# Kernel tuning notes

Hardware: AMD Instinct MI355X
Metric: run time of the kernel (lower is better)

The kernel has to match this reference:

```python
import jax, jax.numpy as jnp
import numpy as np
import math

B, T, D, S, V = 128, 32, 64, 32, 8192
MAX_REC = 8
PONDER = 0.01
TWO_PI = 2.0 * math.pi


def setup_inputs():
    key = jax.random.key(0)
    ks = jax.random.split(key, 12)
    sd = 1.0 / math.sqrt(D)
    g = lambda k, shape, s: jax.random.normal(k, shape, jnp.float32) * s
    return {
        "x_seq": jax.random.randint(ks[0], (B, T), 0, V),
        "encoder_emb": g(ks[1], (V, 2 * D), 0.02),
        "vq_emb": g(ks[2], (V, 2 * D), sd),
        "norm_rg": jnp.ones((D,), jnp.float32), "norm_rb": jnp.zeros((D,), jnp.float32),
        "norm_ig": jnp.ones((D,), jnp.float32), "norm_ib": jnp.zeros((D,), jnp.float32),
        "qkv_Wr": g(ks[3], (3, D, D), sd), "qkv_br": g(ks[4], (3, D), sd),
        "qkv_Wi": g(ks[5], (3, D, D), sd), "qkv_bi": g(ks[6], (3, D), sd),
        "gate_w": g(ks[7], (2 * D,), sd), "gate_b": jnp.zeros((), jnp.float32),
        "arb_W": g(ks[8], (3, 2 * D), sd), "arb_b": jnp.zeros((3,), jnp.float32),
        "dec_W": g(ks[9], (V, 2 * D), sd), "dec_b": jnp.zeros((V,), jnp.float32),
        "halt_bias": jnp.asarray(3.0, jnp.float32),
        "input_gate": jnp.asarray(0.0, jnp.float32),
    }


def _ln(x, g, b, eps=1e-5):
    mu = x.mean(-1, keepdims=True)
    var = ((x - mu) ** 2).mean(-1, keepdims=True)
    return (x - mu) * jax.lax.rsqrt(var + eps) * g + b


def _forward(x_seq, encoder_emb, vq_emb, norm_rg, norm_rb, norm_ig, norm_ib,
             qkv_Wr, qkv_br, qkv_Wi, qkv_bi, gate_w, gate_b, arb_W, arb_b,
             dec_W, dec_b, halt_bias, input_gate):
    sg = jax.lax.stop_gradient
    e_sq = (vq_emb ** 2).sum(-1)  # [V]
    alpha = jax.nn.sigmoid(input_gate)
    bias = jax.nn.softplus(halt_bias)

    def clin(xr, xi, Wr, br, Wi, bi):
        # torch ComplexLinear: real = fc_r(xr) - fc_i(xi); imag = fc_r(xi) + fc_i(xr)
        return (xr @ Wr.T + br) - (xi @ Wi.T + bi), (xi @ Wr.T + br) + (xr @ Wi.T + bi)

    def mem_write(gr, gi, mr, mi):
        flat = jnp.concatenate([gr, gi], -1)
        wg = jax.nn.sigmoid(flat @ gate_w + gate_b)[:, None, None]  # [B,1,1]
        shr, shi = jnp.roll(mr, 1, axis=1), jnp.roll(mi, 1, axis=1)
        hr = wg * gr[:, None, :] + (1.0 - wg) * shr[:, :1]
        hi = wg * gi[:, None, :] + (1.0 - wg) * shi[:, :1]
        return jnp.concatenate([hr, shr[:, 1:]], 1), jnp.concatenate([hi, shi[:, 1:]], 1)

    def time_step(carry, xt):
        gw_r, gw_i, mem_r, mem_i = carry
        x_r, x_i = xt
        gw_r = alpha * gw_r + (1.0 - alpha) * x_r
        gw_i = alpha * gw_i + (1.0 - alpha) * x_i
        active = jnp.ones((B,), jnp.float32)
        acc_vq = jnp.zeros((B,), jnp.float32)
        acc_ent = jnp.zeros((B,), jnp.float32)
        acc_pond = jnp.zeros((B,), jnp.float32)
        acc_ph = jnp.zeros((B,), jnp.float32)
        fin_idx = jnp.zeros((B,), jnp.int32)
        prev_ang = jnp.arctan2(gw_i, gw_r)
        for _ in range(MAX_REC):
            cr = _ln(gw_r, norm_rg, norm_rb)
            ci = _ln(gw_i, norm_ig, norm_ib)
            z_flat = jnp.concatenate([cr, ci], -1)  # [B,2D]
            # squared-euclidean scores; argmin identical to cdist argmin
            d2 = (z_flat ** 2).sum(-1, keepdims=True) - 2.0 * (z_flat @ vq_emb.T) + e_sq
            idx = jnp.argmin(d2, -1).astype(jnp.int32)
            z_q = vq_emb[idx]
            vq_loss = ((z_q - sg(z_flat)) ** 2).mean(-1) + 0.25 * ((sg(z_q) - z_flat) ** 2).mean(-1)
            z_st = z_flat + sg(z_q - z_flat)  # straight-through
            counts = jnp.zeros((V,), jnp.float32).at[idx].add(1.0) / B
            entropy = -(counts * jnp.log(counts + 1e-10)).sum()
            v_r, v_i = z_st[:, :D], z_st[:, D:]
            # Hermitian gating
            qr, qi = clin(cr, ci, qkv_Wr[0], qkv_br[0], qkv_Wi[0], qkv_bi[0])
            kr, ki = clin(cr, ci, qkv_Wr[1], qkv_br[1], qkv_Wi[1], qkv_bi[1])
            vr2, vi2 = clin(cr, ci, qkv_Wr[2], qkv_br[2], qkv_Wi[2], qkv_bi[2])
            gate = jax.nn.sigmoid((qr * kr + qi * ki).sum(-1, keepdims=True))
            g_r, g_i = vr2 * gate, vi2 * gate
            # memory read (Re<m, q> attention over slots)
            sim = jnp.einsum('bsd,bd->bs', mem_r, cr) + jnp.einsum('bsd,bd->bs', mem_i, ci)
            attn = jax.nn.softmax(sim, -1)
            m_r = jnp.einsum('bs,bsd->bd', attn, mem_r)
            m_i = jnp.einsum('bs,bsd->bd', attn, mem_i)
            gates = jax.nn.softmax(z_flat @ arb_W.T + arb_b, -1)  # [B,3]
            upd_r = gates[:, 0:1] * g_r + gates[:, 1:2] * m_r + gates[:, 2:3] * v_r
            upd_i = gates[:, 0:1] * g_i + gates[:, 1:2] * m_i + gates[:, 2:3] * v_i
            cand_r = 0.6 * cr + 0.4 * upd_r
            cand_i = 0.6 * ci + 0.4 * upd_i
            ang = jnp.arctan2(cand_i, cand_r)
            diff = jnp.abs(ang - prev_ang)
            diff = jnp.minimum(diff, TWO_PI - diff)
            acc_ph = acc_ph + active * diff.mean(-1)
            prev_ang = ang
            halt_prob = jax.nn.sigmoid(bias - vq_loss)
            should_stop = (halt_prob > 0.5).astype(jnp.float32)
            acc_pond = acc_pond + active * PONDER
            mflat = active > 0.5
            acc_vq = jnp.where(mflat, vq_loss, acc_vq)
            acc_ent = jnp.where(mflat, entropy, acc_ent)
            fin_idx = jnp.where(mflat, idx, fin_idx)
            am = mflat[:, None]
            gw_r = jnp.where(am, cand_r, gw_r)
            gw_i = jnp.where(am, cand_i, gw_i)
            active = active * (1.0 - should_stop)
        mem_r, mem_i = mem_write(gw_r, gw_i, mem_r, mem_i)
        stats_t = jnp.stack([acc_vq.mean(), acc_ent.mean(), acc_pond.mean(), acc_ph.mean()])
        return (gw_r, gw_i, mem_r, mem_i), (gw_r, gw_i, fin_idx, stats_t)

    emb = encoder_emb[x_seq]  # [B,T,2D]
    xr = jnp.transpose(emb[..., :D], (1, 0, 2))  # [T,B,D]
    xi = jnp.transpose(emb[..., D:], (1, 0, 2))
    init = (jnp.zeros((B, D), jnp.float32), jnp.zeros((B, D), jnp.float32),
            jnp.zeros((B, S, D), jnp.float32), jnp.zeros((B, S, D), jnp.float32))
    _, (out_r, out_i, idxs, stats) = jax.lax.scan(time_step, init, (xr, xi))
    out = jnp.concatenate([jnp.transpose(out_r, (1, 0, 2)),
                           jnp.transpose(out_i, (1, 0, 2))], -1)  # [B,T,2D]
    logits = out @ dec_W.T + dec_b  # [B,T,V]
    return logits, stats.sum(0) / T, jnp.transpose(idxs)  # [B,T]


def reference(x_seq, encoder_emb, vq_emb, norm_rg, norm_rb, norm_ig, norm_ib, qkv_Wr, qkv_br, qkv_Wi, qkv_bi, gate_w, gate_b, arb_W, arb_b, dec_W, dec_b, halt_bias, input_gate):
    return _forward(x_seq, encoder_emb, vq_emb, norm_rg, norm_rb, norm_ig, norm_ib,
                    qkv_Wr, qkv_br, qkv_Wi, qkv_bi, gate_w, gate_b, arb_W, arb_b,
                    dec_W, dec_b, halt_bias, input_gate)
```

## Files before the change

kernel.cpp:

```cpp
#include <hip/hip_runtime.h>
#include <math.h>

#define TT 32
#define MAXREC 8
#define NBLK 256
#define NTHR 512

#define OFF_ZBUF   0u
#define OFF_KEYS   65536u
#define OFF_ZDONE  196608u
#define OFF_SDONE  198656u
#define OFF_OUTHB  200704u
#define OFF_RST    1249280u
#define OFF_DWB    1251328u

#define SENT 0x7FFFFFFFu
#define LOGN 33554432u
#define TWO_PI_F 6.283185307179586f

typedef float f32x4 __attribute__((ext_vector_type(4)));
typedef short bf16x8 __attribute__((ext_vector_type(8)));
typedef unsigned long long u64;

__device__ __forceinline__ float wredsum(float v) {
#pragma unroll
  for (int m = 32; m > 0; m >>= 1) v += __shfl_xor(v, m);
  return v;
}

__device__ __forceinline__ u64 shflx64(u64 v, int m) {
  int lo = __shfl_xor((int)(unsigned)(v & 0xffffffffull), m);
  int hi = __shfl_xor((int)(unsigned)(v >> 32), m);
  return ((u64)(unsigned)hi << 32) | (unsigned)lo;
}

__device__ __forceinline__ u64 packkey(float d, unsigned c) {
  unsigned u = __float_as_uint(d);
  u = (u & 0x80000000u) ? ~u : (u | 0x80000000u);
  return ((u64)u << 32) | c;
}
__device__ __forceinline__ float unpackd2(u64 key) {
  unsigned hi = (unsigned)(key >> 32);
  unsigned orig = (hi & 0x80000000u) ? (hi & 0x7fffffffu) : ~hi;
  return __uint_as_float(orig);
}
__device__ __forceinline__ unsigned short f2bf(float f) {
  unsigned u = __float_as_uint(f);
  unsigned r = (u >> 16) & 1u;
  u += 0x7fffu + r;
  return (unsigned short)(u >> 16);
}

__device__ __forceinline__ unsigned ld_coh32(const unsigned* p) {
  unsigned v;
  asm volatile("global_load_dword %0, %1, off sc0 sc1\n\ts_waitcnt vmcnt(0)"
               : "=&v"(v) : "v"(p) : "memory");
  return v;
}
__device__ __forceinline__ void st_coh_f32(float* p, float v) {
  asm volatile("global_store_dword %0, %1, off sc0 sc1" :: "v"(p), "v"(v) : "memory");
}
__device__ __forceinline__ void st_coh32(unsigned* p, unsigned v) {
  asm volatile("global_store_dword %0, %1, off sc0 sc1" :: "v"(p), "v"(v) : "memory");
}
__device__ __forceinline__ void st_coh64(u64* p, u64 v) {
  asm volatile("global_store_dwordx2 %0, %1, off sc0 sc1" :: "v"(p), "v"(v) : "memory");
}
__device__ __forceinline__ void drain_vm() {
  asm volatile("s_waitcnt vmcnt(0)" ::: "memory");
}

__device__ __forceinline__ void ld8w(const float* base,
    unsigned o0, unsigned o1, unsigned o2, unsigned o3,
    unsigned o4, unsigned o5, unsigned o6, unsigned o7,
    f32x4& a0, f32x4& a1, f32x4& a2, f32x4& a3,
    f32x4& a4, f32x4& a5, f32x4& a6, f32x4& a7) {
  asm volatile(
      "global_load_dwordx4 %0, %8, %16 sc0 sc1\n\t"
      "global_load_dwordx4 %1, %9, %16 sc0 sc1\n\t"
      "global_load_dwordx4 %2, %10, %16 sc0 sc1\n\t"
      "global_load_dwordx4 %3, %11, %16 sc0 sc1\n\t"
      "global_load_dwordx4 %4, %12, %16 sc0 sc1\n\t"
      "global_load_dwordx4 %5, %13, %16 sc0 sc1\n\t"
      "global_load_dwordx4 %6, %14, %16 sc0 sc1\n\t"
      "global_load_dwordx4 %7, %15, %16 sc0 sc1\n\t"
      "s_waitcnt vmcnt(0)"
      : "=&v"(a0), "=&v"(a1), "=&v"(a2), "=&v"(a3),
        "=&v"(a4), "=&v"(a5), "=&v"(a6), "=&v"(a7)
      : "v"(o0), "v"(o1), "v"(o2), "v"(o3),
        "v"(o4), "v"(o5), "v"(o6), "v"(o7),
        "s"(base)
      : "memory");
}
__device__ __forceinline__ void ld8x2_issue(const char* base,
    unsigned o0, unsigned o1, unsigned o2, unsigned o3,
    unsigned o4, unsigned o5, unsigned o6, unsigned o7,
    u64& a0, u64& a1, u64& a2, u64& a3, u64& a4, u64& a5, u64& a6, u64& a7) {
  asm volatile(
      "global_load_dwordx2 %0, %8, %16 sc0 sc1\n\t"
      "global_load_dwordx2 %1, %9, %16 sc0 sc1\n\t"
      "global_load_dwordx2 %2, %10, %16 sc0 sc1\n\t"
      "global_load_dwordx2 %3, %11, %16 sc0 sc1\n\t"
      "global_load_dwordx2 %4, %12, %16 sc0 sc1\n\t"
      "global_load_dwordx2 %5, %13, %16 sc0 sc1\n\t"
      "global_load_dwordx2 %6, %14, %16 sc0 sc1\n\t"
      "global_load_dwordx2 %7, %15, %16 sc0 sc1"
      : "=&v"(a0), "=&v"(a1), "=&v"(a2), "=&v"(a3),
        "=&v"(a4), "=&v"(a5), "=&v"(a6), "=&v"(a7)
      : "v"(o0), "v"(o1), "v"(o2), "v"(o3),
        "v"(o4), "v"(o5), "v"(o6), "v"(o7),
        "s"(base)
      : "memory");
}

__global__ __launch_bounds__(512) void sacrsn_init(char* __restrict__ ws) {
  unsigned* zd = (unsigned*)(ws + OFF_ZDONE);
  unsigned* sd = (unsigned*)(ws + OFF_SDONE);
  zd[threadIdx.x] = 0u;
  sd[threadIdx.x] = 0u;
}

__global__ __launch_bounds__(256) void k_prep(const float* __restrict__ dW,
                                              char* __restrict__ ws) {
  unsigned short* dWb = (unsigned short*)(ws + OFF_DWB);
  const int i = (blockIdx.x * 256 + threadIdx.x) * 4;
  float4 v = *(const float4*)(dW + i);
  ushort4 o;
  o.x = f2bf(v.x); o.y = f2bf(v.y); o.z = f2bf(v.z); o.w = f2bf(v.w);
  *(ushort4*)(dWb + i) = o;
}

__global__ __launch_bounds__(NTHR) void sacrsn_main(
    const int* __restrict__ x_seq, const float* __restrict__ enc,
    const float* __restrict__ vqe,
    const float* __restrict__ nrg, const float* __restrict__ nrb,
    const float* __restrict__ nig, const float* __restrict__ nib,
    const float* __restrict__ qWr, const float* __restrict__ qbr,
    const float* __restrict__ qWi, const float* __restrict__ qbi,
    const float* __restrict__ gtw, const float* __restrict__ gtb,
    const float* __restrict__ aW, const float* __restrict__ ab,
    const float* __restrict__ hbp, const float* __restrict__ igp,
    float* __restrict__ dout, char* __restrict__ ws)
{
  float* zbuf = (float*)(ws + OFF_ZBUF);
  u64*   keys = (u64*)(ws + OFF_KEYS);
  unsigned* zdone = (unsigned*)(ws + OFF_ZDONE);
  unsigned* sdone = (unsigned*)(ws + OFF_SDONE);
  unsigned short* outhB = (unsigned short*)(ws + OFF_OUTHB);
  float* rst  = (float*)(ws + OFF_RST);

  const int tid = threadIdx.x;
  const int wv = tid >> 6, ln = tid & 63;
  const int blk = blockIdx.x;
  const bool owner = (blk < 128);

  __shared__ float els[64 * 128];
  __shared__ float zloc[128 * 128];
  __shared__ u64 vtmp[128 * 17];
  __shared__ float esqL[64];
  __shared__ float z2locL[128];
  __shared__ float memLr[32 * 65];
  __shared__ float memLi[32 * 65];
  __shared__ float gwrowL[128], pangL[64], zfmL[128], zqL[128];
  __shared__ float qkL[6][64], simL[32], attnL[32], mrL[64], miL[64];
  __shared__ unsigned idxL[128] __attribute__((aligned(16)));
  __shared__ u64 key128L[128];
  __shared__ float arbWL[3 * 128];
  __shared__ float scalL[8], entpL[2], vqpL[2], wsumL[2];
  __shared__ float accL[4], totL[4];
  __shared__ float dmeanS;
  __shared__ u64 actM[2], actN[2];
  __shared__ unsigned pollOK, pollSent, mfS;

  const float alpha = 1.0f / (1.0f + expf(-igp[0]));
  const float onema = 1.0f - alpha;
  const float hbias = log1pf(expf(hbp[0]));
  const float gtb0 = gtb[0];

  if (!owner) {
    const int s = blk - 128;
#pragma unroll
    for (int j = 0; j < 4; ++j) {
      int f4 = tid + j * NTHR;
      int c = f4 >> 5, k4 = f4 & 31;
      float4 v = *(const float4*)&vqe[((size_t)(s * 64 + c) << 7) + (k4 << 2)];
      *(float4*)&els[(c << 7) + ((k4 ^ (c & 31)) << 2)] = v;
    }
    __syncthreads();
    if (tid < 64) {
      float sm = 0.0f;
#pragma unroll 8
      for (int k4 = 0; k4 < 32; ++k4) {
        float4 v = *(const float4*)&els[(tid << 7) + ((k4 ^ (tid & 31)) << 2)];
        sm = fmaf(v.x, v.x, fmaf(v.y, v.y, fmaf(v.z, v.z, fmaf(v.w, v.w, sm))));
      }
      esqL[tid] = sm;
    }
    __syncthreads();
    unsigned k = 0;
    while (true) {
      bool done = false;
      while (true) {
        if (tid == 0) { pollOK = 1u; pollSent = 1u; }
        __syncthreads();
        if (tid < 128) {
          unsigned v = ld_coh32(&zdone[tid * 4]);
          if ((int)(v - (k + 1u)) < 0) pollOK = 0u;
          if (v != SENT) pollSent = 0u;
        }
        __syncthreads();
        if (pollSent) { done = true; break; }
        if (pollOK) break;
        __builtin_amdgcn_s_sleep(1);
      }
      if (done) break;
      {
        f32x4 a0, a1, a2, a3, a4, a5, a6, a7;
        const unsigned tb = (unsigned)tid * 16u;
        ld8w(zbuf, tb, tb + 8192u, tb + 16384u, tb + 24576u,
             tb + 32768u, tb + 40960u, tb + 49152u, tb + 57344u,
             a0, a1, a2, a3, a4, a5, a6, a7);
        __builtin_amdgcn_sched_barrier(0);
        f32x4 va[8] = {a0, a1, a2, a3, a4, a5, a6, a7};
#pragma unroll
        for (int u = 0; u < 8; ++u) {
          int f4 = u * NTHR + tid;
          int row = f4 >> 5, k4 = f4 & 31;
          *(f32x4*)&zloc[(row << 7) + ((k4 ^ (row & 31)) << 2)] = va[u];
        }
      }
      __syncthreads();
      if (tid < 128) {
        float sm = 0.0f;
#pragma unroll 8
        for (int k4 = 0; k4 < 32; ++k4) {
          float4 q = *(const float4*)&zloc[(tid << 7) + ((k4 ^ (tid & 31)) << 2)];
          sm = fmaf(q.x, q.x, fmaf(q.y, q.y, fmaf(q.z, q.z, fmaf(q.w, q.w, sm))));
        }
        z2locL[tid] = sm;
      }
      const int rt = tid & 31, ct = tid >> 5;
      float acc[4][4];
#pragma unroll
      for (int rr = 0; rr < 4; ++rr)
#pragma unroll
        for (int cc = 0; cc < 4; ++cc) acc[rr][cc] = 0.0f;
#pragma unroll 2
      for (int k4 = 0; k4 < 32; ++k4) {
        float4 zv[4], ev[4];
#pragma unroll
        for (int rr = 0; rr < 4; ++rr)
          zv[rr] = *(const float4*)&zloc[((rt + rr * 32) << 7) + ((k4 ^ rt) << 2)];
#pragma unroll
        for (int cc = 0; cc < 4; ++cc) {
          int cl = ct * 4 + cc;
          ev[cc] = *(const float4*)&els[(cl << 7) + ((k4 ^ (cl & 31)) << 2)];
        }
#pragma unroll
        for (int rr = 0; rr < 4; ++rr)
#pragma unroll
          for (int cc = 0; cc < 4; ++cc)
            acc[rr][cc] = fmaf(zv[rr].x, ev[cc].x, fmaf(zv[rr].y, ev[cc].y,
                          fmaf(zv[rr].z, ev[cc].z, fmaf(zv[rr].w, ev[cc].w, acc[rr][cc]))));
      }
      __syncthreads();
#pragma unroll
      for (int rr = 0; rr < 4; ++rr) {
        const int row = rt + rr * 32;
        const float z2r = z2locL[row];
        u64 key = ~0ull;
#pragma unroll
        for (int cc = 0; cc < 4; ++cc) {
          int cl = ct * 4 + cc;
          float d2 = (z2r - 2.0f * acc[rr][cc]) + esqL[cl];
          u64 pk = packkey(d2, (unsigned)(s * 64 + cl));
          if (pk < key) key = pk;
        }
        vtmp[row * 17 + ct] = key;
      }
      __syncthreads();
      if (tid < 128) {
        u64 kmin = vtmp[tid * 17];
#pragma unroll
        for (int w = 1; w < 16; ++w) { u64 o = vtmp[tid * 17 + w]; if (o < kmin) kmin = o; }
        st_coh64(&keys[(size_t)s * 128 + tid], kmin);
      }
      drain_vm();
      __syncthreads();
      if (tid == 0) st_coh32(&sdone[s * 4], k + 1u);
      k++;
    }
    return;
  }

  float lnG = 0.0f, lnB = 0.0f, gtwv = 0.0f;
  if (tid < 64) { lnG = nrg[tid]; lnB = nrb[tid]; }
  else if (tid < 128) { lnG = nig[tid - 64]; lnB = nib[tid - 64]; }
  if (tid < 128) gtwv = gtw[tid];
  for (int i = tid; i < 32 * 65; i += NTHR) { memLr[i] = 0.0f; memLi[i] = 0.0f; }
  if (tid < 4) { totL[tid] = 0.0f; accL[tid] = 0.0f; }
  if (tid < 2) actM[tid] = ~0ull;
  for (int i = tid; i < 384; i += NTHR) arbWL[i] = aW[i];
  {
    int tok = x_seq[blk * TT];
    if (tid < 128) gwrowL[tid] = onema * enc[((size_t)tok << 7) + tid];
  }
  __syncthreads();
  if (tid < 64) pangL[tid] = atan2f(gwrowL[64 + tid], gwrowL[tid]);
  if (tid < 128) {
    float val = gwrowL[tid];
    float mu = wredsum(val) * 0.015625f;
    float xc = val - mu;
    float vr = wredsum(xc * xc) * 0.015625f;
    float z = xc * (1.0f / sqrtf(vr + 1e-5f)) * lnG + lnB;
    zfmL[tid] = z;
    st_coh_f32(&zbuf[(blk << 7) + tid], z);
  }
  drain_vm();
  __syncthreads();
  if (tid == 0) st_coh32(&zdone[blk * 4], 1u);

  int t = 0, it = 0;
  unsigned k = 0;
  for (;;) {
    float encN = 0.0f;
    {
      int tnext = (t + 1 < TT) ? t + 1 : t;
      if (tid < 128) {
        int tk = x_seq[blk * TT + tnext];
        encN = enc[((size_t)tk << 7) + tid];
      }
    }
    if (tid < 192) {
      const int h = tid >> 6, j = tid & 63;
      const float* wr = qWr + h * 4096 + j * 64;
      const float* wi = qWi + h * 4096 + j * 64;
      float da = 0.0f, db_ = 0.0f, dc = 0.0f, de = 0.0f;
#pragma unroll 4
      for (int d4 = 0; d4 < 64; d4 += 4) {
        float4 wrv = *(const float4*)&wr[d4];
        float4 wiv = *(const float4*)&wi[d4];
        float4 crv = *(const float4*)&zfmL[d4];
        float4 civ = *(const float4*)&zfmL[64 + d4];
        da = fmaf(crv.x, wrv.x, fmaf(crv.y, wrv.y, fmaf(crv.z, wrv.z, fmaf(crv.w, wrv.w, da))));
        db_ = fmaf(civ.x, wiv.x, fmaf(civ.y, wiv.y, fmaf(civ.z, wiv.z, fmaf(civ.w, wiv.w, db_))));
        dc = fmaf(civ.x, wrv.x, fmaf(civ.y, wrv.y, fmaf(civ.z, wrv.z, fmaf(civ.w, wrv.w, dc))));
        de = fmaf(crv.x, wiv.x, fmaf(crv.y, wiv.y, fmaf(crv.z, wiv.z, fmaf(crv.w, wiv.w, de))));
      }
      float brv = qbr[h * 64 + j], biv = qbi[h * 64 + j];
      qkL[2 * h][j] = da + brv - db_ - biv;
      qkL[2 * h + 1][j] = dc + brv + de + biv;
    } else if (tid < 224) {
      const int s2 = tid - 192;
      float a2 = 0.0f;
      for (int d = 0; d < 64; ++d)
        a2 = fmaf(memLr[s2 * 65 + d], zfmL[d], fmaf(memLi[s2 * 65 + d], zfmL[64 + d], a2));
      simL[s2] = a2;
    } else if (tid < 227) {
      const int h = tid - 224;
      float a2 = ab[h];
      for (int k2 = 0; k2 < 128; ++k2) a2 = fmaf(zfmL[k2], arbWL[h * 128 + k2], a2);
      scalL[3 + h] = a2;
    }
    __syncthreads();
    if (tid < 64) {
      float p = fmaf(qkL[0][tid], qkL[2][tid], qkL[1][tid] * qkL[3][tid]);
      p = wredsum(p);
      if (tid == 0) scalL[0] = 1.0f / (1.0f + expf(-p));
    } else if (tid < 96) {
      const int s2 = tid - 64;
      float v = simL[s2];
      float m = v;
#pragma unroll
      for (int msk = 16; msk > 0; msk >>= 1) m = fmaxf(m, __shfl_xor(m, msk));
      float e = expf(v - m);
      float ss = e;
#pragma unroll
      for (int msk = 16; msk > 0; msk >>= 1) ss += __shfl_xor(ss, msk);
      attnL[s2] = e / ss;
    } else if (tid == 96) {
      float a0 = scalL[3], a1 = scalL[4], a2 = scalL[5];
      float m = fmaxf(a0, fmaxf(a1, a2));
      float e0 = expf(a0 - m), e1 = expf(a1 - m), e2 = expf(a2 - m);
      float ssum = e0 + e1 + e2;
      scalL[3] = e0 / ssum; scalL[4] = e1 / ssum; scalL[5] = e2 / ssum;
    }
    __syncthreads();
    if (tid < 128) {
      const int d = ln;
      const float* ml = (wv == 0) ? memLr : memLi;
      float a2 = 0.0f;
#pragma unroll 4
      for (int s2 = 0; s2 < 32; ++s2) a2 = fmaf(attnL[s2], ml[s2 * 65 + d], a2);
      if (wv == 0) mrL[d] = a2; else miL[d] = a2;
    }
    while (true) {
      if (tid == 0) pollOK = 1u;
      __syncthreads();
      if (tid < 128) {
        unsigned v = ld_coh32(&sdone[tid * 4]);
        if ((int)(v - (k + 1u)) < 0) pollOK = 0u;
      }
      __syncthreads();
      if (pollOK) break;
      __builtin_amdgcn_s_sleep(1);
    }
    {
      const int r = tid >> 2, sc = tid & 3;
      const char* kb = (const char*)keys;
      const unsigned bo = (unsigned)(sc * 32768 + r * 8);
      u64 g00, g01, g02, g03, g04, g05, g06, g07;
      u64 g10, g11, g12, g13, g14, g15, g16, g17;
      u64 g20, g21, g22, g23, g24, g25, g26, g27;
      u64 g30, g31, g32, g33, g34, g35, g36, g37;
      ld8x2_issue(kb, bo, bo + 1024u, bo + 2048u, bo + 3072u,
                  bo + 4096u, bo + 5120u, bo + 6144u, bo + 7168u,
                  g00, g01, g02, g03, g04, g05, g06, g07);
      ld8x2_issue(kb, bo + 8192u, bo + 9216u, bo + 10240u, bo + 11264u,
                  bo + 12288u, bo + 13312u, bo + 14336u, bo + 15360u,
                  g10, g11, g12, g13, g14, g15, g16, g17);
      ld8x2_issue(kb, bo + 16384u, bo + 17408u, bo + 18432u, bo + 19456u,
                  bo + 20480u, bo + 21504u, bo + 22528u, bo + 23552u,
                  g20, g21, g22, g23, g24, g25, g26, g27);
      ld8x2_issue(kb, bo + 24576u, bo + 25600u, bo + 26624u, bo + 27648u,
                  bo + 28672u, bo + 29696u, bo + 30720u, bo + 31744u,
                  g30, g31, g32, g33, g34, g35, g36, g37);
      drain_vm();
      __builtin_amdgcn_sched_barrier(0);
      u64 m = g00;
      if (g01 < m) m = g01; if (g02 < m) m = g02; if (g03 < m) m = g03;
      if (g04 < m) m = g04; if (g05 < m) m = g05; if (g06 < m) m = g06; if (g07 < m) m = g07;
      if (g10 < m) m = g10; if (g11 < m) m = g11; if (g12 < m) m = g12; if (g13 < m) m = g13;
      if (g14 < m) m = g14; if (g15 < m) m = g15; if (g16 < m) m = g16; if (g17 < m) m = g17;
      if (g20 < m) m = g20; if (g21 < m) m = g21; if (g22 < m) m = g22; if (g23 < m) m = g23;
      if (g24 < m) m = g24; if (g25 < m) m = g25; if (g26 < m) m = g26; if (g27 < m) m = g27;
      if (g30 < m) m = g30; if (g31 < m) m = g31; if (g32 < m) m = g32; if (g33 < m) m = g33;
      if (g34 < m) m = g34; if (g35 < m) m = g35; if (g36 < m) m = g36; if (g37 < m) m = g37;
      u64 o = shflx64(m, 1); if (o < m) m = o;
      o = shflx64(m, 2); if (o < m) m = o;
      if (sc == 0) key128L[r] = m;
    }
    __syncthreads();
    if (tid < 128) {
      u64 key = key128L[tid];
      idxL[tid] = (unsigned)key;
      float d2 = unpackd2(key);
      bool act_b = ((actM[tid >> 6] >> (tid & 63)) & 1ull) != 0ull;
      bool stop = (1.25f * 0.0078125f * d2) < hbias;
      u64 ball = __ballot(act_b && !stop);
      if (ln == 0) actN[tid >> 6] = ball;
    }
    __syncthreads();
    if (tid == 0) mfS = (unsigned)((actM[blk >> 6] >> (blk & 63)) & 1ull);
    if (tid < 2) actM[tid] = actN[tid];
    __syncthreads();
    const bool anyAct = (actN[0] | actN[1]) != 0ull;
    const bool mf = mfS != 0u;
    const unsigned ii = idxL[blk];
    if (tid < 128) {
      float zq = vqe[((size_t)ii << 7) + tid];
      zqL[tid] = zq;
      float df = zq - zfmL[tid];
      float sm = wredsum(df * df);
      if (ln == 0) vqpL[wv] = sm;
    } else if (tid < 256) {
      const int r = tid - 128;
      unsigned my = idxL[r];
      int c = 0;
#pragma unroll
      for (int j4 = 0; j4 < 32; ++j4) {
        uint4 q = *(const uint4*)&idxL[j4 * 4];
        c += (q.x == my) + (q.y == my) + (q.z == my) + (q.w == my);
      }
      float term = -0.0078125f * logf((float)c * 0.0078125f + 1e-10f);
      term = wredsum(term);
      if (ln == 0) entpL[wv - 2] = term;
    }
    __syncthreads();
    if (tid < 64) {
      const int d = tid;
      float gate = scalL[0], g0 = scalL[3], g1 = scalL[4], g2 = scalL[5];
      float cr = zfmL[d], ci = zfmL[64 + d];
      float ur = fmaf(g0, qkL[4][d] * gate, fmaf(g1, mrL[d], g2 * zqL[d]));
      float ui = fmaf(g0, qkL[5][d] * gate, fmaf(g1, miL[d], g2 * zqL[64 + d]));
      float cdr = fmaf(0.4f, ur, 0.6f * cr);
      float cdi = fmaf(0.4f, ui, 0.6f * ci);
      float ang = atan2f(cdi, cdr);
      float df = fabsf(ang - pangL[d]);
      df = fminf(df, TWO_PI_F - df);
      pangL[d] = ang;
      float dm = wredsum(df) * 0.015625f;
      if (mf) { gwrowL[d] = cdr; gwrowL[64 + d] = cdi; }
      if (d == 0) dmeanS = dm;
    }
    __syncthreads();
    const bool newT = !(anyAct && it < MAXREC - 1);
    const bool finished = newT && (t == TT - 1);
    if (newT && !finished) {
      float pr = 0.0f;
      if (tid < 128) {
        pr = gwrowL[tid];
        outhB[((size_t)blk * TT + t) * 128 + tid] = f2bf(pr);
        float part = wredsum(pr * gtwv);
        if (ln == 0) wsumL[wv] = part;
      }
      __syncthreads();
      if (tid < 128) {
        float wg = 1.0f / (1.0f + expf(-(wsumL[0] + wsumL[1] + gtb0)));
        int slot = 31 - t;
        float* m = (tid < 64) ? &memLr[slot * 65 + tid] : &memLi[slot * 65 + (tid - 64)];
        *m = fmaf(wg, pr, (1.0f - wg) * (*m));
        gwrowL[tid] = fmaf(alpha, pr, onema * encN);
      }
      __syncthreads();
    }
    if (!finished) {
      if (tid < 128) {
        float val = gwrowL[tid];
        float mu = wredsum(val) * 0.015625f;
        float xc = val - mu;
        float vr = wredsum(xc * xc) * 0.015625f;
        float z = xc * (1.0f / sqrtf(vr + 1e-5f)) * lnG + lnB;
        zfmL[tid] = z;
        st_coh_f32(&zbuf[(blk << 7) + tid], z);
      }
      drain_vm();
      __syncthreads();
      if (tid == 0) st_coh32(&zdone[blk * 4], k + 2u);
    } else {
      __syncthreads();
    }
    if (tid == 0) {
      float aold = mf ? 1.0f : 0.0f;
      float vql = 1.25f * (vqpL[0] + vqpL[1]) * 0.0078125f;
      accL[3] += aold * dmeanS;
      accL[2] += aold * 0.01f;
      if (mf) {
        accL[0] = vql;
        accL[1] = entpL[0] + entpL[1];
        dout[(size_t)LOGN + 4 + (size_t)blk * TT + t] = (float)ii;
      }
    }
    if (newT && !finished) {
      if (tid < 64) pangL[tid] = atan2f(gwrowL[64 + tid], gwrowL[tid]);
      if (tid < 4) { totL[tid] += accL[tid]; accL[tid] = 0.0f; }
      if (tid < 2) actM[tid] = ~0ull;
    }
    __syncthreads();
    if (finished) break;
    if (newT) { t++; it = 0; } else { it++; }
    k++;
  }

  if (tid < 128) outhB[((size_t)blk * TT + (TT - 1)) * 128 + tid] = f2bf(gwrowL[tid]);
  if (tid < 4) rst[blk * 4 + tid] = totL[tid] + accL[tid];
  __syncthreads();
  if (tid == 0) st_coh32(&zdone[blk * 4], SENT);
}

__global__ __launch_bounds__(256) void k_dec(
    const float* __restrict__ dbv, float* __restrict__ dout,
    const char* __restrict__ ws)
{
  const unsigned short* outhB = (const unsigned short*)(ws + OFF_OUTHB);
  const unsigned short* dWb = (const unsigned short*)(ws + OFF_DWB);
  const float* rst = (const float*)(ws + OFF_RST);
  const int tid = threadIdx.x;
  if (blockIdx.x == 0 && tid < 4) {
    float s = 0.0f;
    for (int r = 0; r < 128; ++r) s += rst[r * 4 + tid];
    dout[(size_t)LOGN + tid] = s * (1.0f / 4096.0f);
  }
  const int w = tid >> 6, l = tid & 63;
  const int bm = blockIdx.x & 63;
  const int bn = blockIdx.x >> 6;
  const int ar = l & 15, kg = l >> 4;
  const int m_base = bm * 64;
  const int n_base = bn * 256 + w * 64;
  f32x4 acc[4][4];
#pragma unroll
  for (int mt = 0; mt < 4; ++mt)
#pragma unroll
    for (int nt = 0; nt < 4; ++nt) acc[mt][nt] = (f32x4){0.f, 0.f, 0.f, 0.f};
#pragma unroll
  for (int kc = 0; kc < 4; ++kc) {
    const int ko = kc * 32 + kg * 8;
    bf16x8 a[4], b[4];
#pragma unroll
    for (int mt = 0; mt < 4; ++mt)
      a[mt] = *(const bf16x8*)(outhB + (size_t)(m_base + mt * 16 + ar) * 128 + ko);
#pragma unroll
    for (int nt = 0; nt < 4; ++nt)
      b[nt] = *(const bf16x8*)(dWb + (size_t)(n_base + nt * 16 + ar) * 128 + ko);
#pragma unroll
    for (int mt = 0; mt < 4; ++mt)
#pragma unroll
      for (int nt = 0; nt < 4; ++nt)
        acc[mt][nt] = __builtin_amdgcn_mfma_f32_16x16x32_bf16(a[mt], b[nt], acc[mt][nt], 0, 0, 0);
  }
#pragma unroll
  for (int nt = 0; nt < 4; ++nt) {
    const int n = n_base + nt * 16 + ar;
    const float bv = dbv[n];
#pragma unroll
    for (int mt = 0; mt < 4; ++mt) {
#pragma unroll
      for (int rr = 0; rr < 4; ++rr) {
        const int m = m_base + mt * 16 + kg * 4 + rr;
        dout[(size_t)m * 8192 + n] = acc[mt][nt][rr] + bv;
      }
    }
  }
}

extern "C" void kernel_launch(void* const* d_in, const int* in_sizes, int n_in,
                              void* d_out, int out_size, void* d_ws, size_t ws_size,
                              hipStream_t stream) {
  (void)in_sizes; (void)n_in; (void)out_size; (void)ws_size;
  const int*   x_seq = (const int*)d_in[0];
  const float* enc = (const float*)d_in[1];
  const float* vq  = (const float*)d_in[2];
  const float* nrg = (const float*)d_in[3];
  const float* nrb = (const float*)d_in[4];
  const float* nig = (const float*)d_in[5];
  const float* nib = (const float*)d_in[6];
  const float* qWr = (const float*)d_in[7];
  const float* qbr = (const float*)d_in[8];
  const float* qWi = (const float*)d_in[9];
  const float* qbi = (const float*)d_in[10];
  const float* gtw = (const float*)d_in[11];
  const float* gtb = (const float*)d_in[12];
  const float* aW  = (const float*)d_in[13];
  const float* ab  = (const float*)d_in[14];
  const float* dW  = (const float*)d_in[15];
  const float* db  = (const float*)d_in[16];
  const float* hb  = (const float*)d_in[17];
  const float* ig  = (const float*)d_in[18];
  char* ws = (char*)d_ws;
  float* out = (float*)d_out;
  hipLaunchKernelGGL(sacrsn_init, dim3(1), dim3(512), 0, stream, ws);
  hipLaunchKernelGGL(k_prep, dim3(1024), dim3(256), 0, stream, dW, ws);
  hipLaunchKernelGGL(sacrsn_main, dim3(NBLK), dim3(NTHR), 0, stream,
                     x_seq, enc, vq, nrg, nrb, nig, nib, qWr, qbr, qWi, qbi,
                     gtw, gtb, aW, ab, hb, ig, out, ws);
  hipLaunchKernelGGL(k_dec, dim3(2048), dim3(256), 0, stream, db, out, ws);
}
```

Baseline: 817.5 us.

## Embed step tags in key words and split argmin into distributed per-owner reductions

Worker blocks now write each partial argmin key with the iteration tag packed into bits above the index, and stop issuing a separate done-flag store behind a drain and barrier. Each owner block polls only its own column of keys, reduces it to a final key, publishes that through a small tagged array, and then polls all 128 finals. This replaces the flag-then-bulk-load protocol with tagged data that doubles as the ready signal. Block size is also doubled to 1024 threads with a reshaped distance tile. The trade is a second cross-block polling round and the assumption that the index and tag bits fit below the distance bits.

```diff
diff --git a/kernel.cpp b/kernel.cpp
--- a/kernel.cpp
+++ b/kernel.cpp
@@ -4,17 +4,18 @@
 #define TT 32
 #define MAXREC 8
 #define NBLK 256
-#define NTHR 512
+#define NTHR 1024
 
 #define OFF_ZBUF   0u
 #define OFF_KEYS   65536u
 #define OFF_ZDONE  196608u
-#define OFF_SDONE  198656u
+#define OFF_FINAL  198656u
 #define OFF_OUTHB  200704u
 #define OFF_RST    1249280u
 #define OFF_DWB    1251328u
 
 #define SENT 0x7FFFFFFFu
+#define IDXM 0x1FFFu
 #define LOGN 33554432u
 #define TWO_PI_F 6.283185307179586f
 
@@ -57,6 +58,12 @@
                : "=&v"(v) : "v"(p) : "memory");
   return v;
 }
+__device__ __forceinline__ u64 ld_coh64(const u64* p) {
+  u64 v;
+  asm volatile("global_load_dwordx2 %0, %1, off sc0 sc1\n\ts_waitcnt vmcnt(0)"
+               : "=&v"(v) : "v"(p) : "memory");
+  return v;
+}
 __device__ __forceinline__ void st_coh_f32(float* p, float v) {
   asm volatile("global_store_dword %0, %1, off sc0 sc1" :: "v"(p), "v"(v) : "memory");
 }
@@ -70,54 +77,25 @@
   asm volatile("s_waitcnt vmcnt(0)" ::: "memory");
 }
 
-__device__ __forceinline__ void ld8w(const float* base,
+__device__ __forceinline__ void ld4w(const float* base,
     unsigned o0, unsigned o1, unsigned o2, unsigned o3,
-    unsigned o4, unsigned o5, unsigned o6, unsigned o7,
-    f32x4& a0, f32x4& a1, f32x4& a2, f32x4& a3,
-    f32x4& a4, f32x4& a5, f32x4& a6, f32x4& a7) {
+    f32x4& a0, f32x4& a1, f32x4& a2, f32x4& a3) {
   asm volatile(
-      "global_load_dwordx4 %0, %8, %16 sc0 sc1\n\t"
-      "global_load_dwordx4 %1, %9, %16 sc0 sc1\n\t"
-      "global_load_dwordx4 %2, %10, %16 sc0 sc1\n\t"
-      "global_load_dwordx4 %3, %11, %16 sc0 sc1\n\t"
-      "global_load_dwordx4 %4, %12, %16 sc0 sc1\n\t"
-      "global_load_dwordx4 %5, %13, %16 sc0 sc1\n\t"
-      "global_load_dwordx4 %6, %14, %16 sc0 sc1\n\t"
-      "global_load_dwordx4 %7, %15, %16 sc0 sc1\n\t"
+      "global_load_dwordx4 %0, %4, %8 sc0 sc1\n\t"
+      "global_load_dwordx4 %1, %5, %8 sc0 sc1\n\t"
+      "global_load_dwordx4 %2, %6, %8 sc0 sc1\n\t"
+      "global_load_dwordx4 %3, %7, %8 sc0 sc1\n\t"
       "s_waitcnt vmcnt(0)"
-      : "=&v"(a0), "=&v"(a1), "=&v"(a2), "=&v"(a3),
-        "=&v"(a4), "=&v"(a5), "=&v"(a6), "=&v"(a7)
-      : "v"(o0), "v"(o1), "v"(o2), "v"(o3),
-        "v"(o4), "v"(o5), "v"(o6), "v"(o7),
-        "s"(base)
-      : "memory");
-}
-__device__ __forceinline__ void ld8x2_issue(const char* base,
-    unsigned o0, unsigned o1, unsigned o2, unsigned o3,
-    unsigned o4, unsigned o5, unsigned o6, unsigned o7,
-    u64& a0, u64& a1, u64& a2, u64& a3, u64& a4, u64& a5, u64& a6, u64& a7) {
-  asm volatile(
-      "global_load_dwordx2 %0, %8, %16 sc0 sc1\n\t"
-      "global_load_dwordx2 %1, %9, %16 sc0 sc1\n\t"
-      "global_load_dwordx2 %2, %10, %16 sc0 sc1\n\t"
-      "global_load_dwordx2 %3, %11, %16 sc0 sc1\n\t"
-      "global_load_dwordx2 %4, %12, %16 sc0 sc1\n\t"
-      "global_load_dwordx2 %5, %13, %16 sc0 sc1\n\t"
-      "global_load_dwordx2 %6, %14, %16 sc0 sc1\n\t"
-      "global_load_dwordx2 %7, %15, %16 sc0 sc1"
-      : "=&v"(a0), "=&v"(a1), "=&v"(a2), "=&v"(a3),
-        "=&v"(a4), "=&v"(a5), "=&v"(a6), "=&v"(a7)
-      : "v"(o0), "v"(o1), "v"(o2), "v"(o3),
-        "v"(o4), "v"(o5), "v"(o6), "v"(o7),
-        "s"(base)
+      : "=&v"(a0), "=&v"(a1), "=&v"(a2), "=&v"(a3)
+      : "v"(o0), "v"(o1), "v"(o2), "v"(o3), "s"(base)
       : "memory");
 }
 
 __global__ __launch_bounds__(512) void sacrsn_init(char* __restrict__ ws) {
   unsigned* zd = (unsigned*)(ws + OFF_ZDONE);
-  unsigned* sd = (unsigned*)(ws + OFF_SDONE);
+  u64* fin = (u64*)(ws + OFF_FINAL);
   zd[threadIdx.x] = 0u;
-  sd[threadIdx.x] = 0u;
+  if (threadIdx.x < 128) fin[threadIdx.x] = 0ull;
 }
 
 __global__ __launch_bounds__(256) void k_prep(const float* __restrict__ dW,
@@ -145,7 +123,7 @@
   float* zbuf = (float*)(ws + OFF_ZBUF);
   u64*   keys = (u64*)(ws + OFF_KEYS);
   unsigned* zdone = (unsigned*)(ws + OFF_ZDONE);
-  unsigned* sdone = (unsigned*)(ws + OFF_SDONE);
+  u64*   finalA = (u64*)(ws + OFF_FINAL);
   unsigned short* outhB = (unsigned short*)(ws + OFF_OUTHB);
   float* rst  = (float*)(ws + OFF_RST);
 
@@ -164,7 +142,7 @@
   __shared__ float gwrowL[128], pangL[64], zfmL[128], zqL[128];
   __shared__ float qkL[6][64], simL[32], attnL[32], mrL[64], miL[64];
   __shared__ unsigned idxL[128] __attribute__((aligned(16)));
-  __shared__ u64 key128L[128];
+  __shared__ u64 key128L[128], kred[128];
   __shared__ float arbWL[3 * 128];
   __shared__ float scalL[8], entpL[2], vqpL[2], wsumL[2];
   __shared__ float accL[4], totL[4];
@@ -180,7 +158,7 @@
   if (!owner) {
     const int s = blk - 128;
 #pragma unroll
-    for (int j = 0; j < 4; ++j) {
+    for (int j = 0; j < 2; ++j) {
       int f4 = tid + j * NTHR;
       int c = f4 >> 5, k4 = f4 & 31;
       float4 v = *(const float4*)&vqe[((size_t)(s * 64 + c) << 7) + (k4 << 2)];
@@ -215,15 +193,13 @@
       }
       if (done) break;
       {
-        f32x4 a0, a1, a2, a3, a4, a5, a6, a7;
+        f32x4 a0, a1, a2, a3;
         const unsigned tb = (unsigned)tid * 16u;
-        ld8w(zbuf, tb, tb + 8192u, tb + 16384u, tb + 24576u,
-             tb + 32768u, tb + 40960u, tb + 49152u, tb + 57344u,
-             a0, a1, a2, a3, a4, a5, a6, a7);
+        ld4w(zbuf, tb, tb + 16384u, tb + 32768u, tb + 49152u, a0, a1, a2, a3);
         __builtin_amdgcn_sched_barrier(0);
-        f32x4 va[8] = {a0, a1, a2, a3, a4, a5, a6, a7};
-#pragma unroll
-        for (int u = 0; u < 8; ++u) {
+        f32x4 va[4] = {a0, a1, a2, a3};
+#pragma unroll
+        for (int u = 0; u < 4; ++u) {
           int f4 = u * NTHR + tid;
           int row = f4 >> 5, k4 = f4 & 31;
           *(f32x4*)&zloc[(row << 7) + ((k4 ^ (row & 31)) << 2)] = va[u];
@@ -239,25 +215,25 @@
         }
         z2locL[tid] = sm;
       }
-      const int rt = tid & 31, ct = tid >> 5;
-      float acc[4][4];
-#pragma unroll
-      for (int rr = 0; rr < 4; ++rr)
+      const int rt = tid & 63, ct = tid >> 6;
+      float acc[2][4];
+#pragma unroll
+      for (int rr = 0; rr < 2; ++rr)
 #pragma unroll
         for (int cc = 0; cc < 4; ++cc) acc[rr][cc] = 0.0f;
 #pragma unroll 2
       for (int k4 = 0; k4 < 32; ++k4) {
-        float4 zv[4], ev[4];
-#pragma unroll
-        for (int rr = 0; rr < 4; ++rr)
-          zv[rr] = *(const float4*)&zloc[((rt + rr * 32) << 7) + ((k4 ^ rt) << 2)];
+        float4 zv[2], ev[4];
+#pragma unroll
+        for (int rr = 0; rr < 2; ++rr)
+          zv[rr] = *(const float4*)&zloc[((rt + rr * 64) << 7) + ((k4 ^ (rt & 31)) << 2)];
 #pragma unroll
         for (int cc = 0; cc < 4; ++cc) {
           int cl = ct * 4 + cc;
           ev[cc] = *(const float4*)&els[(cl << 7) + ((k4 ^ (cl & 31)) << 2)];
         }
 #pragma unroll
-        for (int rr = 0; rr < 4; ++rr)
+        for (int rr = 0; rr < 2; ++rr)
 #pragma unroll
           for (int cc = 0; cc < 4; ++cc)
             acc[rr][cc] = fmaf(zv[rr].x, ev[cc].x, fmaf(zv[rr].y, ev[cc].y,
@@ -265,8 +241,8 @@
       }
       __syncthreads();
 #pragma unroll
-      for (int rr = 0; rr < 4; ++rr) {
-        const int row = rt + rr * 32;
+      for (int rr = 0; rr < 2; ++rr) {
+        const int row = rt + rr * 64;
         const float z2r = z2locL[row];
         u64 key = ~0ull;
 #pragma unroll
@@ -283,11 +259,8 @@
         u64 kmin = vtmp[tid * 17];
 #pragma unroll
         for (int w = 1; w < 16; ++w) { u64 o = vtmp[tid * 17 + w]; if (o < kmin) kmin = o; }
-        st_coh64(&keys[(size_t)s * 128 + tid], kmin);
-      }
-      drain_vm();
-      __syncthreads();
-      if (tid == 0) st_coh32(&sdone[s * 4], k + 1u);
+        st_coh64(&keys[(size_t)s * 128 + tid], kmin | ((u64)(k + 1u) << 13));
+      }
       k++;
     }
     return;
@@ -323,6 +296,7 @@
   int t = 0, it = 0;
   unsigned k = 0;
   for (;;) {
+    const unsigned tag = k + 1u;
     float encN = 0.0f;
     {
       int tnext = (t + 1 < TT) ? t + 1 : t;
@@ -398,52 +372,36 @@
       if (tid == 0) pollOK = 1u;
       __syncthreads();
       if (tid < 128) {
-        unsigned v = ld_coh32(&sdone[tid * 4]);
-        if ((int)(v - (k + 1u)) < 0) pollOK = 0u;
+        u64 v = ld_coh64(&keys[(size_t)tid * 128 + blk]);
+        if ((unsigned)((v >> 13) & 0x7FFFFull) != tag) pollOK = 0u;
+        else kred[tid] = v;
       }
       __syncthreads();
       if (pollOK) break;
       __builtin_amdgcn_s_sleep(1);
     }
-    {
-      const int r = tid >> 2, sc = tid & 3;
-      const char* kb = (const char*)keys;
-      const unsigned bo = (unsigned)(sc * 32768 + r * 8);
-      u64 g00, g01, g02, g03, g04, g05, g06, g07;
-      u64 g10, g11, g12, g13, g14, g15, g16, g17;
-      u64 g20, g21, g22, g23, g24, g25, g26, g27;
-      u64 g30, g31, g32, g33, g34, g35, g36, g37;
-      ld8x2_issue(kb, bo, bo + 1024u, bo + 2048u, bo + 3072u,
-                  bo + 4096u, bo + 5120u, bo + 6144u, bo + 7168u,
-                  g00, g01, g02, g03, g04, g05, g06, g07);
-      ld8x2_issue(kb, bo + 8192u, bo + 9216u, bo + 10240u, bo + 11264u,
-                  bo + 12288u, bo + 13312u, bo + 14336u, bo + 15360u,
-                  g10, g11, g12, g13, g14, g15, g16, g17);
-      ld8x2_issue(kb, bo + 16384u, bo + 17408u, bo + 18432u, bo + 19456u,
-                  bo + 20480u, bo + 21504u, bo + 22528u, bo + 23552u,
-                  g20, g21, g22, g23, g24, g25, g26, g27);
-      ld8x2_issue(kb, bo + 24576u, bo + 25600u, bo + 26624u, bo + 27648u,
-                  bo + 28672u, bo + 29696u, bo + 30720u, bo + 31744u,
-                  g30, g31, g32, g33, g34, g35, g36, g37);
-      drain_vm();
-      __builtin_amdgcn_sched_barrier(0);
-      u64 m = g00;
-      if (g01 < m) m = g01; if (g02 < m) m = g02; if (g03 < m) m = g03;
-      if (g04 < m) m = g04; if (g05 < m) m = g05; if (g06 < m) m = g06; if (g07 < m) m = g07;
-      if (g10 < m) m = g10; if (g11 < m) m = g11; if (g12 < m) m = g12; if (g13 < m) m = g13;
-      if (g14 < m) m = g14; if (g15 < m) m = g15; if (g16 < m) m = g16; if (g17 < m) m = g17;
-      if (g20 < m) m = g20; if (g21 < m) m = g21; if (g22 < m) m = g22; if (g23 < m) m = g23;
-      if (g24 < m) m = g24; if (g25 < m) m = g25; if (g26 < m) m = g26; if (g27 < m) m = g27;
-      if (g30 < m) m = g30; if (g31 < m) m = g31; if (g32 < m) m = g32; if (g33 < m) m = g33;
-      if (g34 < m) m = g34; if (g35 < m) m = g35; if (g36 < m) m = g36; if (g37 < m) m = g37;
-      u64 o = shflx64(m, 1); if (o < m) m = o;
-      o = shflx64(m, 2); if (o < m) m = o;
-      if (sc == 0) key128L[r] = m;
-    }
-    __syncthreads();
+    if (tid < 64) {
+      u64 a = kred[tid], b = kred[tid + 64];
+      if (b < a) a = b;
+#pragma unroll
+      for (int m2 = 32; m2 > 0; m2 >>= 1) { u64 o = shflx64(a, m2); if (o < a) a = o; }
+      if (tid == 0) st_coh64(&finalA[blk], a);
+    }
+    while (true) {
+      if (tid == 0) pollOK = 1u;
+      __syncthreads();
+      if (tid < 128) {
+        u64 v = ld_coh64(&finalA[tid]);
+        if ((unsigned)((v >> 13) & 0x7FFFFull) != tag) pollOK = 0u;
+        else key128L[tid] = v;
+      }
+      __syncthreads();
+      if (pollOK) break;
+      __builtin_amdgcn_s_sleep(1);
+    }
     if (tid < 128) {
       u64 key = key128L[tid];
-      idxL[tid] = (unsigned)key;
+      idxL[tid] = (unsigned)key & IDXM;
       float d2 = unpackd2(key);
       bool act_b = ((actM[tid >> 6] >> (tid & 63)) & 1ull) != 0ull;
       bool stop = (1.25f * 0.0078125f * d2) < hbias;
```

New measurement: 738.8 us. -9.6%, faster.
